# Optimization experiments

Hardware: AMD Instinct MI355X
Metric: run time of the kernel (lower is better)

The kernel has to match this reference:

```python
import jax, jax.numpy as jnp
import numpy as np

N_SAMPLES = 16384
SPB = 1024            # samples_per_block
ROOM = (16, 16, 16)   # room_dim
MIC = (8, 8, 8)       # mic_location
ENV_SIZE = 16         # impulse_envelope_size
N_BLOCKS = N_SAMPLES // SPB
N_COEFFS = SPB // 2 + 1


def _linear_interp(env, out_size):
    # torch F.interpolate(mode='linear', align_corners=False) along last axis
    in_size = env.shape[-1]
    scale = in_size / out_size
    coords = jnp.clip((jnp.arange(out_size, dtype=jnp.float32) + 0.5) * scale - 0.5,
                      0.0, in_size - 1.0)
    lo = jnp.floor(coords).astype(jnp.int32)
    hi = jnp.minimum(lo + 1, in_size - 1)
    w = coords - lo.astype(jnp.float32)
    return env[..., lo] * (1.0 - w) + env[..., hi] * w


def setup_inputs() -> dict:
    key = jax.random.key(0)
    k1, k2, k3, k4 = jax.random.split(key, 4)
    x = jax.random.normal(k1, (1, 1, N_SAMPLES), dtype=jnp.float32)  # unused by forward
    transfer_functions = jax.random.uniform(k2, (N_BLOCKS, *ROOM, N_COEFFS), dtype=jnp.float32)
    impulses = jax.random.uniform(k3, (N_BLOCKS, *ROOM, ENV_SIZE), dtype=jnp.float32)
    # the torch forward draws U(-1,1) noise each block; hoisted here as an input
    noise = jax.random.uniform(k4, (N_BLOCKS, *ROOM, SPB), minval=-1.0, maxval=1.0,
                               dtype=jnp.float32)
    return {"x": x, "transfer_functions": transfer_functions,
            "impulses": impulses, "noise": noise}


def reference(x, transfer_functions, impulses, noise):
    # Precompute per-block excitation envelopes: interp -> clamp -> * noise
    env = jnp.clip(_linear_interp(impulses, SPB), 0.0, 1.0) * noise  # (B, X, Y, Z, T)
    res = jnp.clip(transfer_functions, 0.0, 1.0)                      # (B, X, Y, Z, F)

    def step(sound_field, blk):
        e, r = blk
        sf = sound_field + e
        spec = jnp.fft.rfft(sf, axis=-1, norm='ortho')
        sf = jnp.fft.irfft(r * spec, n=SPB, axis=-1, norm='ortho')
        mic = sf[MIC[0], MIC[1], MIC[2]]                              # (T,)
        # 3x3x3 ones-kernel box sum over spatial dims, zero padding 1 (== unfold path)
        sf = jax.lax.reduce_window(sf, 0.0, jax.lax.add,
                                   (3, 3, 3, 1), (1, 1, 1, 1), 'SAME')
        return sf, mic

    sf0 = jnp.zeros((*ROOM, SPB), dtype=jnp.float32)
    _, mics = jax.lax.scan(step, sf0, (env, res))                     # mics: (B, T)
    return mics.reshape(-1, 1, N_SAMPLES)                             # (1, 1, n_samples)
```

## Files before the change

### kernel.cpp

```cpp
#include <hip/hip_runtime.h>


#define NFFT   1024
#define NF     513
#define NKP    257
#define NCELLS 4096
#define NPAIR  2048
#define PI2    6.28318530717958647692f
#define RT2    0.70710678118654752f

__device__ __forceinline__ int SW(int i) {
    return i ^ ((i >> 4) & 7) ^ ((i >> 7) & 7);
}
__device__ __forceinline__ int slotof(int k) {
    return ((k & 7) << 7) | (((k >> 3) & 7) << 4) | (((k >> 6) & 7) << 1) | ((k >> 9) & 1);
}
__device__ __forceinline__ float clip01(float v) { return fminf(fmaxf(v, 0.0f), 1.0f); }
__device__ __forceinline__ unsigned pkh2(float a, float b) {
    union { _Float16 h[2]; unsigned u; } z;
    z.h[0] = (_Float16)a; z.h[1] = (_Float16)b;
    return z.u;
}
__device__ __forceinline__ float h2lo(unsigned u) {
    union { unsigned u; _Float16 h[2]; } z; z.u = u; return (float)z.h[0];
}
__device__ __forceinline__ float h2hi(unsigned u) {
    union { unsigned u; _Float16 h[2]; } z; z.u = u; return (float)z.h[1];
}
__device__ __forceinline__ unsigned cmp4(const uint4& v, int c) {
    return c == 0 ? v.x : c == 1 ? v.y : c == 2 ? v.z : v.w;
}
__device__ __forceinline__ float4 f4add(float4 a, float4 b) {
    return make_float4(a.x + b.x, a.y + b.y, a.z + b.z, a.w + b.w);
}
__device__ __forceinline__ float4 f4sub(float4 a, float4 b) {
    return make_float4(a.x - b.x, a.y - b.y, a.z - b.z, a.w - b.w);
}
__device__ __forceinline__ float4 cmul2(float4 d, float2 w) {
    return make_float4(d.x * w.x - d.y * w.y, d.x * w.y + d.y * w.x,
                       d.z * w.x - d.w * w.y, d.z * w.y + d.w * w.x);
}
__device__ __forceinline__ float4 nI(float4 v) { return make_float4(v.y, -v.x, v.w, -v.z); }
__device__ __forceinline__ float4 pI(float4 v) { return make_float4(-v.y, v.x, -v.w, v.z); }
__device__ __forceinline__ float4 w81(float4 v) {
    return make_float4(RT2 * (v.x + v.y), RT2 * (v.y - v.x),
                       RT2 * (v.z + v.w), RT2 * (v.w - v.z));
}
__device__ __forceinline__ float4 w83(float4 v) {
    return make_float4(RT2 * (v.y - v.x), RT2 * (-v.x - v.y),
                       RT2 * (v.w - v.z), RT2 * (-v.z - v.w));
}

__device__ __forceinline__ void dft8(float4* a) {
    float4 c0 = f4add(a[0], a[4]), c1 = f4add(a[1], a[5]);
    float4 c2 = f4add(a[2], a[6]), c3 = f4add(a[3], a[7]);
    float4 d0 = f4sub(a[0], a[4]);
    float4 d1 = w81(f4sub(a[1], a[5]));
    float4 d2 = nI (f4sub(a[2], a[6]));
    float4 d3 = w83(f4sub(a[3], a[7]));
    float4 t0 = f4add(c0, c2), t1 = f4add(c1, c3);
    float4 t2 = f4sub(c0, c2), t3 = f4sub(c1, c3);
    float4 s0 = f4add(d0, d2), s1 = f4add(d1, d3);
    float4 s2 = f4sub(d0, d2), s3 = f4sub(d1, d3);
    a[0] = f4add(t0, t1);      a[4] = f4sub(t0, t1);
    a[2] = f4add(t2, nI(t3));  a[6] = f4add(t2, pI(t3));
    a[1] = f4add(s0, s1);      a[5] = f4sub(s0, s1);
    a[3] = f4add(s2, nI(s3));  a[7] = f4add(s2, pI(s3));
}

__device__ __forceinline__ void twiddle7(float4* a, int j, float invL) {
    float sv, cv;
    __sincosf(-PI2 * (float)j * invL, &sv, &cv);
    float2 w1 = make_float2(cv, sv), wp = w1;
    a[1] = cmul2(a[1], wp);
    #pragma unroll
    for (int p = 2; p < 8; ++p) {
        wp = make_float2(wp.x * w1.x - wp.y * w1.y, wp.x * w1.y + wp.y * w1.x);
        a[p] = cmul2(a[p], wp);
    }
}

__global__ __launch_bounds__(256, 5) void k_p1(
    const float* __restrict__ tf, const float* __restrict__ imp,
    const float* __restrict__ noise, unsigned* __restrict__ Et,
    unsigned* __restrict__ TFt)
{
    __shared__ float4 FD[2][1024];

    const int tid = threadIdx.x;
    const int bid = blockIdx.x;
    const int w   = ((bid & 7) << 10) | (bid >> 3);
    const int b   = w >> 9;
    const int c0  = (w & 511) << 3;
    const int buf = tid >> 7, j1 = tid & 127;
    const int cb  = c0 + 4 * buf;

    {
        const float* nz = noise + ((size_t)b * NCELLS + cb) * (size_t)NFFT;
        float nzv[32];
        #pragma unroll
        for (int m = 0; m < 8; ++m) {
            #pragma unroll
            for (int cc = 0; cc < 4; ++cc)
                nzv[4 * m + cc] = nz[cc * NFFT + j1 + (m << 7)];
        }
        const float* ipr = imp + ((size_t)b * NCELLS + cb) * 16;
        float4 a[8];
        #pragma unroll
        for (int m = 0; m < 8; ++m) {
            int n = j1 + (m << 7);
            float coord = (n + 0.5f) * (16.0f / 1024.0f) - 0.5f;
            coord = fminf(fmaxf(coord, 0.0f), 15.0f);
            int lo = (int)coord;
            int hi = lo + 1 > 15 ? 15 : lo + 1;
            float wl = coord - (float)lo, wh = 1.0f - wl;
            float4 e;
            e.x = clip01(ipr[lo]      * wh + ipr[hi]      * wl) * nzv[4 * m + 0];
            e.y = clip01(ipr[16 + lo] * wh + ipr[16 + hi] * wl) * nzv[4 * m + 1];
            e.z = clip01(ipr[32 + lo] * wh + ipr[32 + hi] * wl) * nzv[4 * m + 2];
            e.w = clip01(ipr[48 + lo] * wh + ipr[48 + hi] * wl) * nzv[4 * m + 3];
            a[m] = e;
        }
        dft8(a);
        twiddle7(a, j1, 1.0f / 1024.0f);
        #pragma unroll
        for (int p = 0; p < 8; ++p) FD[buf][SW(j1 + (p << 7))] = a[p];
    }
    __syncthreads();

    {
        const int idx0 = ((j1 >> 4) << 7) + (j1 & 15);
        float4 a[8];
        #pragma unroll
        for (int m = 0; m < 8; ++m) a[m] = FD[buf][SW(idx0 + (m << 4))];
        dft8(a);
        twiddle7(a, j1 & 15, 1.0f / 128.0f);
        #pragma unroll
        for (int p = 0; p < 8; ++p) FD[buf][SW(idx0 + (p << 4))] = a[p];
    }
    __syncthreads();

    {
        const int idx0 = ((j1 >> 1) << 4) + (j1 & 1);
        float4 a[8];
        #pragma unroll
        for (int m = 0; m < 8; ++m) a[m] = FD[buf][SW(idx0 + (m << 1))];
        dft8(a);
        twiddle7(a, j1 & 1, 1.0f / 16.0f);
        #pragma unroll
        for (int p = 0; p < 8; ++p) FD[buf][SW(idx0 + (p << 1))] = a[p];
    }
    __syncthreads();

    #pragma unroll
    for (int it = 0; it < 2; ++it) {
        int p = tid + (it << 8);
        float4 A0 = FD[0][SW(2 * p)], B0 = FD[0][SW(2 * p + 1)];
        float4 A1 = FD[1][SW(2 * p)], B1 = FD[1][SW(2 * p + 1)];
        float4 y00 = f4add(A0, B0), y10 = f4sub(A0, B0);
        float4 y01 = f4add(A1, B1), y11 = f4sub(A1, B1);
        uint4 u0 = { pkh2(y00.x, y00.y), pkh2(y00.z, y00.w),
                     pkh2(y01.x, y01.y), pkh2(y01.z, y01.w) };
        uint4 u1 = { pkh2(y10.x, y10.y), pkh2(y10.z, y10.w),
                     pkh2(y11.x, y11.y), pkh2(y11.z, y11.w) };
        unsigned* base = Et + ((size_t)b * NFFT + 2 * p) * NPAIR + (c0 >> 1);
        *(uint4*)base = u0;
        *(uint4*)(base + NPAIR) = u1;
    }

    {
        const float* r_[8];
        #pragma unroll
        for (int cc = 0; cc < 8; ++cc)
            r_[cc] = tf + ((size_t)b * NCELLS + c0 + cc) * NF;
        for (int kp = tid; kp < NKP; kp += 256) {
            bool hv = kp < 256;
            uint4 ua, ub;
            ua.x = pkh2(clip01(r_[0][2 * kp]), hv ? clip01(r_[0][2 * kp + 1]) : 0.0f);
            ua.y = pkh2(clip01(r_[1][2 * kp]), hv ? clip01(r_[1][2 * kp + 1]) : 0.0f);
            ua.z = pkh2(clip01(r_[2][2 * kp]), hv ? clip01(r_[2][2 * kp + 1]) : 0.0f);
            ua.w = pkh2(clip01(r_[3][2 * kp]), hv ? clip01(r_[3][2 * kp + 1]) : 0.0f);
            ub.x = pkh2(clip01(r_[4][2 * kp]), hv ? clip01(r_[4][2 * kp + 1]) : 0.0f);
            ub.y = pkh2(clip01(r_[5][2 * kp]), hv ? clip01(r_[5][2 * kp + 1]) : 0.0f);
            ub.z = pkh2(clip01(r_[6][2 * kp]), hv ? clip01(r_[6][2 * kp + 1]) : 0.0f);
            ub.w = pkh2(clip01(r_[7][2 * kp]), hv ? clip01(r_[7][2 * kp + 1]) : 0.0f);
            unsigned* dst = TFt + ((size_t)b * NKP + kp) * NCELLS + c0;
            *(uint4*)dst = ua;
            *(uint4*)(dst + 4) = ub;
        }
    }
}

__global__ __launch_bounds__(1024, 8) void k_p2(
    const unsigned* __restrict__ Et, const unsigned* __restrict__ TFt,
    float2* __restrict__ ms)
{
    __shared__ float2 Sz[4096];

    const int q    = threadIdx.x;
    const int lane = q & 63;
    const int k    = blockIdx.x;
    const bool dual = (k == 0);
    const int kp  = dual ? 0 : (k >> 1);
    const int sel = dual ? 0 : (k & 1);
    const int rA  = dual ? 0 : slotof(k);
    const int rB  = dual ? 1 : slotof((1024 - k) & 1023);
    const int x = q >> 6, y = (q >> 2) & 15, zs = (q & 3) << 2;

    #define AX(qq, dz) (((qq) << 2) | ((dz) ^ ((qq) & 3) ^ (((qq) >> 2) & 3)))

    float2 SF[4];
    #pragma unroll
    for (int dz = 0; dz < 4; ++dz) SF[dz] = make_float2(0.f, 0.f);

    #pragma unroll 1
    for (int b = 0; b < 16; ++b) {
        const uint2 ea = *(const uint2*)(Et + ((size_t)b * NFFT + rA) * NPAIR + 2 * q);
        const uint2 eb = *(const uint2*)(Et + ((size_t)b * NFFT + rB) * NPAIR + 2 * q);
        const uint4 tp = *(const uint4*)(TFt + ((size_t)b * NKP + kp) * NCELLS + 4 * q);
        uint4 tp2;
        if (dual) tp2 = *(const uint4*)(TFt + ((size_t)b * NKP + 256) * NCELLS + 4 * q);

        float2 T[4];
        if (!dual) {
            #pragma unroll
            for (int j = 0; j < 2; ++j) {
                unsigned fu = j ? ea.y : ea.x;
                unsigned gu = j ? eb.y : eb.x;
                float fr = h2lo(fu), fi = h2hi(fu);
                float gr = h2lo(gu), gi = h2hi(gu);
                float ear = 0.5f * (fr + gr), eai = 0.5f * (fi - gi);
                float ebr = 0.5f * (fi + gi), ebi = 0.5f * (gr - fr);
                unsigned te = cmp4(tp, 2 * j);
                unsigned to = cmp4(tp, 2 * j + 1);
                float re_ = sel ? h2hi(te) : h2lo(te);
                float ro_ = sel ? h2hi(to) : h2lo(to);
                T[2 * j]     = make_float2(re_ * (SF[2 * j].x + ear),
                                           re_ * (SF[2 * j].y + eai));
                T[2 * j + 1] = make_float2(ro_ * (SF[2 * j + 1].x + ebr),
                                           ro_ * (SF[2 * j + 1].y + ebi));
            }
        } else {
            #pragma unroll
            for (int dz = 0; dz < 4; ++dz) {
                unsigned fu = (dz >> 1) ? ea.y : ea.x;
                unsigned gu = (dz >> 1) ? eb.y : eb.x;
                float e0   = (dz & 1) ? h2hi(fu) : h2lo(fu);
                float e512 = (dz & 1) ? h2hi(gu) : h2lo(gu);
                float tA = h2lo(cmp4(tp, dz));
                float tB = h2lo(cmp4(tp2, dz));
                T[dz] = make_float2(tA * (SF[dz].x + e0),
                                    tB * (SF[dz].y + e512));
            }
        }
        if (q == 546) {
            if (dual) {
                ms[b * NF + 0]   = make_float2(T[0].x, 0.0f);
                ms[b * NF + 512] = make_float2(T[0].y, 0.0f);
            } else {
                ms[b * NF + k] = T[0];
            }
        }

        float2 D, U;
        D.x = __shfl(T[3].x, lane - 1, 64); D.y = __shfl(T[3].y, lane - 1, 64);
        U.x = __shfl(T[0].x, lane + 1, 64); U.y = __shfl(T[0].y, lane + 1, 64);
        float2 Z[4];
        Z[0] = make_float2(T[0].x + T[1].x + (zs > 0 ? D.x : 0.f),
                           T[0].y + T[1].y + (zs > 0 ? D.y : 0.f));
        Z[1] = make_float2(T[0].x + T[1].x + T[2].x, T[0].y + T[1].y + T[2].y);
        Z[2] = make_float2(T[1].x + T[2].x + T[3].x, T[1].y + T[2].y + T[3].y);
        Z[3] = make_float2(T[2].x + T[3].x + (zs < 12 ? U.x : 0.f),
                           T[2].y + T[3].y + (zs < 12 ? U.y : 0.f));

        #pragma unroll
        for (int dz = 0; dz < 4; ++dz) Sz[AX(q, dz)] = Z[dz];
        __syncthreads();
        #pragma unroll
        for (int dz = 0; dz < 4; ++dz) {
            float2 s = Z[dz];
            if (y > 0)  { float2 u = Sz[AX(q - 4, dz)]; s.x += u.x; s.y += u.y; }
            if (y < 15) { float2 u = Sz[AX(q + 4, dz)]; s.x += u.x; s.y += u.y; }
            Z[dz] = s;
        }
        __syncthreads();
        #pragma unroll
        for (int dz = 0; dz < 4; ++dz) Sz[AX(q, dz)] = Z[dz];
        __syncthreads();
        #pragma unroll
        for (int dz = 0; dz < 4; ++dz) {
            float2 s = Z[dz];
            if (x > 0)  { float2 u = Sz[AX(q - 64, dz)]; s.x += u.x; s.y += u.y; }
            if (x < 15) { float2 u = Sz[AX(q + 64, dz)]; s.x += u.x; s.y += u.y; }
            SF[dz] = s;
        }
        __syncthreads();
    }
    #undef AX
}

__device__ __forceinline__ int pd(int i) { return i + (i >> 5); }

__global__ __launch_bounds__(256) void k_p3(
    const float2* __restrict__ ms, float* __restrict__ out)
{
    __shared__ float2 FD[1056];
    const int b = blockIdx.x, tid = threadIdx.x;

    for (int j = tid; j < NFFT; j += 256) {
        int jj = (j <= 512) ? j : 1024 - j;
        float2 v = ms[b * NF + jj];
        if (j > 512) v.y = -v.y;
        FD[pd(__brev(j) >> 22)] = v;
    }
    __syncthreads();

    for (int lg = 0; lg <= 9; ++lg) {
        const int len = 1 << lg;
        for (int pr = tid; pr < 512; pr += 256) {
            const int jj = pr & (len - 1);
            const int i0 = ((pr >> lg) << (lg + 1)) + jj;
            const int i1 = i0 + len;
            const int iw = jj << (9 - lg);
            float sn, cs;
            __sincosf(-PI2 * (1.0f / 1024.0f) * (float)iw, &sn, &cs);
            float2 a = FD[pd(i0)], bb = FD[pd(i1)];
            float tr = bb.x * cs + bb.y * sn;
            float ti = bb.y * cs - bb.x * sn;
            FD[pd(i0)] = make_float2(a.x + tr, a.y + ti);
            FD[pd(i1)] = make_float2(a.x - tr, a.y - ti);
        }
        __syncthreads();
    }
    for (int t = tid; t < NFFT; t += 256)
        out[b * NFFT + t] = FD[pd(t)].x * (1.0f / 1024.0f);
}

extern "C" void kernel_launch(void* const* d_in, const int* in_sizes, int n_in,
                              void* d_out, int out_size, void* d_ws, size_t ws_size,
                              hipStream_t stream)
{
    const float* tf    = (const float*)d_in[1];
    const float* imp   = (const float*)d_in[2];
    const float* noise = (const float*)d_in[3];
    float* out = (float*)d_out;

    unsigned* Et  = (unsigned*)d_ws;
    unsigned* TFt = Et + (size_t)16 * NFFT * NPAIR;
    float2*   ms  = (float2*)(TFt + (size_t)16 * NKP * NCELLS);

    k_p1<<<8192, 256, 0, stream>>>(tf, imp, noise, Et, TFt);
    k_p2<<<512, 1024, 0, stream>>>(Et, TFt, ms);
    k_p3<<<16, 256, 0, stream>>>(ms, out);
}
```

Measured before the change: 264.4 us.

## Stage FFT output in shared memory and write Et in contiguous cell-chunk layout

Each k_p1 block now handles 16 cells, in two passes of 8, instead of 8. Spectra are staged in a padded shared-memory buffer, and Et is rewritten into a chunked layout [b][cellchunk][freq][8] so each block writes one contiguous 32KB region instead of scattered 16-byte pieces across rows. k_p2 indexing is updated to match. The cost is fewer blocks, more shared memory (occupancy hint cut from 5 to 2), and k_p2 reads that are now less contiguous per wavefront (8-byte pieces spread across chunks).

```diff
diff --git a/kernel.cpp b/kernel.cpp
--- a/kernel.cpp
+++ b/kernel.cpp
@@ -5,7 +5,6 @@
 #define NF     513
 #define NKP    257
 #define NCELLS 4096
-#define NPAIR  2048
 #define PI2    6.28318530717958647692f
 #define RT2    0.70710678118654752f
 
@@ -80,113 +79,146 @@
     }
 }
 
-__global__ __launch_bounds__(256, 5) void k_p1(
+__global__ __launch_bounds__(256, 2) void k_p1(
     const float* __restrict__ tf, const float* __restrict__ imp,
     const float* __restrict__ noise, unsigned* __restrict__ Et,
     unsigned* __restrict__ TFt)
 {
     __shared__ float4 FD[2][1024];
+    __shared__ unsigned stag[1024 * 9];
 
     const int tid = threadIdx.x;
     const int bid = blockIdx.x;
-    const int w   = ((bid & 7) << 10) | (bid >> 3);
-    const int b   = w >> 9;
-    const int c0  = (w & 511) << 3;
+    const int w   = ((bid & 7) << 9) | (bid >> 3);
+    const int b   = w >> 8;
+    const int c0  = (w & 255) << 4;
     const int buf = tid >> 7, j1 = tid & 127;
-    const int cb  = c0 + 4 * buf;
-
+
+    float2 tu0[3], tu1[3], tl[3];
     {
-        const float* nz = noise + ((size_t)b * NCELLS + cb) * (size_t)NFFT;
-        float nzv[32];
-        #pragma unroll
-        for (int m = 0; m < 8; ++m) {
-            #pragma unroll
-            for (int cc = 0; cc < 4; ++cc)
-                nzv[4 * m + cc] = nz[cc * NFFT + j1 + (m << 7)];
-        }
-        const float* ipr = imp + ((size_t)b * NCELLS + cb) * 16;
-        float4 a[8];
-        #pragma unroll
-        for (int m = 0; m < 8; ++m) {
-            int n = j1 + (m << 7);
-            float coord = (n + 0.5f) * (16.0f / 1024.0f) - 0.5f;
-            coord = fminf(fmaxf(coord, 0.0f), 15.0f);
-            int lo = (int)coord;
-            int hi = lo + 1 > 15 ? 15 : lo + 1;
-            float wl = coord - (float)lo, wh = 1.0f - wl;
-            float4 e;
-            e.x = clip01(ipr[lo]      * wh + ipr[hi]      * wl) * nzv[4 * m + 0];
-            e.y = clip01(ipr[16 + lo] * wh + ipr[16 + hi] * wl) * nzv[4 * m + 1];
-            e.z = clip01(ipr[32 + lo] * wh + ipr[32 + hi] * wl) * nzv[4 * m + 2];
-            e.w = clip01(ipr[48 + lo] * wh + ipr[48 + hi] * wl) * nzv[4 * m + 3];
-            a[m] = e;
-        }
-        dft8(a);
-        twiddle7(a, j1, 1.0f / 1024.0f);
-        #pragma unroll
-        for (int p = 0; p < 8; ++p) FD[buf][SW(j1 + (p << 7))] = a[p];
+        float s, c;
+        __sincosf(-PI2 * (1.0f / 1024.0f) * (float)j1, &s, &c);           tu0[0] = make_float2(c, s);
+        __sincosf(-PI2 * (1.0f / 1024.0f) * (float)(j1 & 15), &s, &c);
+        tu0[1] = make_float2(c, s);
+        __sincosf(-PI2 * (1.0f / 1024.0f) * (float)(j1 & 1), &s, &c);
+        tu0[2] = make_float2(c, s);
+    }
+
+    #pragma unroll 1
+    for (int bb = 0; bb < 2; ++bb) {
+        const int cb = c0 + 8 * bb + 4 * buf;
+        if (bb) __syncthreads();
+
+        {
+            const float* nz = noise + ((size_t)b * NCELLS + cb) * (size_t)NFFT;
+            float nzv[32];
+            #pragma unroll
+            for (int m = 0; m < 8; ++m) {
+                #pragma unroll
+                for (int cc = 0; cc < 4; ++cc)
+                    nzv[4 * m + cc] = nz[cc * NFFT + j1 + (m << 7)];
+            }
+            const float* ipr = imp + ((size_t)b * NCELLS + cb) * 16;
+            float4 a[8];
+            #pragma unroll
+            for (int m = 0; m < 8; ++m) {
+                int n = j1 + (m << 7);
+                float coord = (n + 0.5f) * (16.0f / 1024.0f) - 0.5f;
+                coord = fminf(fmaxf(coord, 0.0f), 15.0f);
+                int lo = (int)coord;
+                int hi = lo + 1 > 15 ? 15 : lo + 1;
+                float wl = coord - (float)lo, wh = 1.0f - wl;
+                float4 e;
+                e.x = clip01(ipr[lo]      * wh + ipr[hi]      * wl) * nzv[4 * m + 0];
+                e.y = clip01(ipr[16 + lo] * wh + ipr[16 + hi] * wl) * nzv[4 * m + 1];
+                e.z = clip01(ipr[32 + lo] * wh + ipr[32 + hi] * wl) * nzv[4 * m + 2];
+                e.w = clip01(ipr[48 + lo] * wh + ipr[48 + hi] * wl) * nzv[4 * m + 3];
+                a[m] = e;
+            }
+            dft8(a);
+            twiddle7(a, j1, 1.0f / 1024.0f);
+            #pragma unroll
+            for (int p = 0; p < 8; ++p) FD[buf][SW(j1 + (p << 7))] = a[p];
+        }
+        __syncthreads();
+
+        {
+            const int idx0 = ((j1 >> 4) << 7) + (j1 & 15);
+            float4 a[8];
+            #pragma unroll
+            for (int m = 0; m < 8; ++m) a[m] = FD[buf][SW(idx0 + (m << 4))];
+            dft8(a);
+            twiddle7(a, j1 & 15, 1.0f / 128.0f);
+            #pragma unroll
+            for (int p = 0; p < 8; ++p) FD[buf][SW(idx0 + (p << 4))] = a[p];
+        }
+        __syncthreads();
+
+        {
+            const int idx0 = ((j1 >> 1) << 4) + (j1 & 1);
+            float4 a[8];
+            #pragma unroll
+            for (int m = 0; m < 8; ++m) a[m] = FD[buf][SW(idx0 + (m << 1))];
+            dft8(a);
+            twiddle7(a, j1 & 1, 1.0f / 16.0f);
+            #pragma unroll
+            for (int p = 0; p < 8; ++p) FD[buf][SW(idx0 + (p << 1))] = a[p];
+        }
+        __syncthreads();
+
+        #pragma unroll
+        for (int it = 0; it < 2; ++it) {
+            int p = tid + (it << 8);
+            float4 A0 = FD[0][SW(2 * p)], B0 = FD[0][SW(2 * p + 1)];
+            float4 A1 = FD[1][SW(2 * p)], B1 = FD[1][SW(2 * p + 1)];
+            float4 y00 = f4add(A0, B0), y10 = f4sub(A0, B0);
+            float4 y01 = f4add(A1, B1), y11 = f4sub(A1, B1);
+            int r0 = (2 * p) * 9 + 4 * bb;
+            int r1 = (2 * p + 1) * 9 + 4 * bb;
+            stag[r0 + 0] = pkh2(y00.x, y00.y);
+            stag[r0 + 1] = pkh2(y00.z, y00.w);
+            stag[r0 + 2] = pkh2(y01.x, y01.y);
+            stag[r0 + 3] = pkh2(y01.z, y01.w);
+            stag[r1 + 0] = pkh2(y10.x, y10.y);
+            stag[r1 + 1] = pkh2(y10.z, y10.w);
+            stag[r1 + 2] = pkh2(y11.x, y11.y);
+            stag[r1 + 3] = pkh2(y11.z, y11.w);
+        }
     }
     __syncthreads();
 
     {
-        const int idx0 = ((j1 >> 4) << 7) + (j1 & 15);
-        float4 a[8];
-        #pragma unroll
-        for (int m = 0; m < 8; ++m) a[m] = FD[buf][SW(idx0 + (m << 4))];
-        dft8(a);
-        twiddle7(a, j1 & 15, 1.0f / 128.0f);
-        #pragma unroll
-        for (int p = 0; p < 8; ++p) FD[buf][SW(idx0 + (p << 4))] = a[p];
-    }
-    __syncthreads();
+        unsigned* base = Et + (((size_t)b * 256 + (c0 >> 4)) * 1024) * 8;
+        #pragma unroll
+        for (int it = 0; it < 4; ++it) {
+            int s = tid + (it << 8);
+            uint4 lo = { stag[s * 9 + 0], stag[s * 9 + 1], stag[s * 9 + 2], stag[s * 9 + 3] };
+            uint4 hi = { stag[s * 9 + 4], stag[s * 9 + 5], stag[s * 9 + 6], stag[s * 9 + 7] };
+            *(uint4*)(base + (size_t)s * 8)     = lo;
+            *(uint4*)(base + (size_t)s * 8 + 4) = hi;
+        }
+    }
 
     {
-        const int idx0 = ((j1 >> 1) << 4) + (j1 & 1);
-        float4 a[8];
-        #pragma unroll
-        for (int m = 0; m < 8; ++m) a[m] = FD[buf][SW(idx0 + (m << 1))];
-        dft8(a);
-        twiddle7(a, j1 & 1, 1.0f / 16.0f);
-        #pragma unroll
-        for (int p = 0; p < 8; ++p) FD[buf][SW(idx0 + (p << 1))] = a[p];
-    }
-    __syncthreads();
-
-    #pragma unroll
-    for (int it = 0; it < 2; ++it) {
-        int p = tid + (it << 8);
-        float4 A0 = FD[0][SW(2 * p)], B0 = FD[0][SW(2 * p + 1)];
-        float4 A1 = FD[1][SW(2 * p)], B1 = FD[1][SW(2 * p + 1)];
-        float4 y00 = f4add(A0, B0), y10 = f4sub(A0, B0);
-        float4 y01 = f4add(A1, B1), y11 = f4sub(A1, B1);
-        uint4 u0 = { pkh2(y00.x, y00.y), pkh2(y00.z, y00.w),
-                     pkh2(y01.x, y01.y), pkh2(y01.z, y01.w) };
-        uint4 u1 = { pkh2(y10.x, y10.y), pkh2(y10.z, y10.w),
-                     pkh2(y11.x, y11.y), pkh2(y11.z, y11.w) };
-        unsigned* base = Et + ((size_t)b * NFFT + 2 * p) * NPAIR + (c0 >> 1);
-        *(uint4*)base = u0;
-        *(uint4*)(base + NPAIR) = u1;
-    }
-
-    {
-        const float* r_[8];
-        #pragma unroll
-        for (int cc = 0; cc < 8; ++cc)
-            r_[cc] = tf + ((size_t)b * NCELLS + c0 + cc) * NF;
+        const float* rbase = tf + ((size_t)b * NCELLS + c0) * NF;
         for (int kp = tid; kp < NKP; kp += 256) {
             bool hv = kp < 256;
-            uint4 ua, ub;
-            ua.x = pkh2(clip01(r_[0][2 * kp]), hv ? clip01(r_[0][2 * kp + 1]) : 0.0f);
-            ua.y = pkh2(clip01(r_[1][2 * kp]), hv ? clip01(r_[1][2 * kp + 1]) : 0.0f);
-            ua.z = pkh2(clip01(r_[2][2 * kp]), hv ? clip01(r_[2][2 * kp + 1]) : 0.0f);
-            ua.w = pkh2(clip01(r_[3][2 * kp]), hv ? clip01(r_[3][2 * kp + 1]) : 0.0f);
-            ub.x = pkh2(clip01(r_[4][2 * kp]), hv ? clip01(r_[4][2 * kp + 1]) : 0.0f);
-            ub.y = pkh2(clip01(r_[5][2 * kp]), hv ? clip01(r_[5][2 * kp + 1]) : 0.0f);
-            ub.z = pkh2(clip01(r_[6][2 * kp]), hv ? clip01(r_[6][2 * kp + 1]) : 0.0f);
-            ub.w = pkh2(clip01(r_[7][2 * kp]), hv ? clip01(r_[7][2 * kp + 1]) : 0.0f);
+            uint4 u[4];
+            #pragma unroll
+            for (int g = 0; g < 4; ++g) {
+                unsigned vv[4];
+                #pragma unroll
+                for (int cq = 0; cq < 4; ++cq) {
+                    const float* rr = rbase + (size_t)(4 * g + cq) * NF;
+                    vv[cq] = pkh2(clip01(rr[2 * kp]), hv ? clip01(rr[2 * kp + 1]) : 0.0f);
+                }
+                u[g] = make_uint4(vv[0], vv[1], vv[2], vv[3]);
+            }
             unsigned* dst = TFt + ((size_t)b * NKP + kp) * NCELLS + c0;
-            *(uint4*)dst = ua;
-            *(uint4*)(dst + 4) = ub;
+            *(uint4*)(dst)      = u[0];
+            *(uint4*)(dst + 4)  = u[1];
+            *(uint4*)(dst + 8)  = u[2];
+            *(uint4*)(dst + 12) = u[3];
         }
     }
 }
@@ -215,8 +247,9 @@
 
     #pragma unroll 1
     for (int b = 0; b < 16; ++b) {
-        const uint2 ea = *(const uint2*)(Et + ((size_t)b * NFFT + rA) * NPAIR + 2 * q);
-        const uint2 eb = *(const uint2*)(Et + ((size_t)b * NFFT + rB) * NPAIR + 2 * q);
+        const size_t chunkbase = ((size_t)b * 256 + (q >> 2)) * 1024;
+        const uint2 ea = *(const uint2*)(Et + (chunkbase + rA) * 8 + 2 * (q & 3));
+        const uint2 eb = *(const uint2*)(Et + (chunkbase + rB) * 8 + 2 * (q & 3));
         const uint4 tp = *(const uint4*)(TFt + ((size_t)b * NKP + kp) * NCELLS + 4 * q);
         uint4 tp2;
         if (dual) tp2 = *(const uint4*)(TFt + ((size_t)b * NKP + 256) * NCELLS + 4 * q);
@@ -346,10 +379,10 @@
     float* out = (float*)d_out;
 
     unsigned* Et  = (unsigned*)d_ws;
-    unsigned* TFt = Et + (size_t)16 * NFFT * NPAIR;
+    unsigned* TFt = Et + (size_t)16 * 256 * 1024 * 8;
     float2*   ms  = (float2*)(TFt + (size_t)16 * NKP * NCELLS);
 
-    k_p1<<<8192, 256, 0, stream>>>(tf, imp, noise, Et, TFt);
+    k_p1<<<4096, 256, 0, stream>>>(tf, imp, noise, Et, TFt);
     k_p2<<<512, 1024, 0, stream>>>(Et, TFt, ms);
     k_p3<<<16, 256, 0, stream>>>(ms, out);
 }
```

New measurement: 313.1 us. 18.4% more time.

## Switch forward FFT to radix-4 with one 4-cell group per block

Applied to the files above, without the earlier changes.

The first-stage kernel moves from a 3-pass radix-8 FFT (two 4-cell groups per 256-thread block, with a final radix-2 pass) to a 5-pass radix-4 FFT over a single 4-cell group per block. The block count doubles, the shared-memory buffer halves and the XOR swizzle is dropped. The output slot mapping changes to a base-4 digit reversal, and the consumer kernel's index function is updated to match. The aim is higher occupancy and lower register pressure in exchange for more passes and barriers, possible unswizzled LDS bank conflicts, and narrower scattered global stores.

```diff
diff --git a/kernel.cpp b/kernel.cpp
--- a/kernel.cpp
+++ b/kernel.cpp
@@ -7,13 +7,10 @@
 #define NCELLS 4096
 #define NPAIR  2048
 #define PI2    6.28318530717958647692f
-#define RT2    0.70710678118654752f
-
-__device__ __forceinline__ int SW(int i) {
-    return i ^ ((i >> 4) & 7) ^ ((i >> 7) & 7);
-}
-__device__ __forceinline__ int slotof(int k) {
-    return ((k & 7) << 7) | (((k >> 3) & 7) << 4) | (((k >> 6) & 7) << 1) | ((k >> 9) & 1);
+
+__device__ __forceinline__ int slotof4(int k) {
+    return ((k & 3) << 8) | (((k >> 2) & 3) << 6) | (((k >> 4) & 3) << 4) |
+           (((k >> 6) & 3) << 2) | ((k >> 8) & 3);
 }
 __device__ __forceinline__ float clip01(float v) { return fminf(fmaxf(v, 0.0f), 1.0f); }
 __device__ __forceinline__ unsigned pkh2(float a, float b) {
@@ -42,73 +39,54 @@
 }
 __device__ __forceinline__ float4 nI(float4 v) { return make_float4(v.y, -v.x, v.w, -v.z); }
 __device__ __forceinline__ float4 pI(float4 v) { return make_float4(-v.y, v.x, -v.w, v.z); }
-__device__ __forceinline__ float4 w81(float4 v) {
-    return make_float4(RT2 * (v.x + v.y), RT2 * (v.y - v.x),
-                       RT2 * (v.z + v.w), RT2 * (v.w - v.z));
-}
-__device__ __forceinline__ float4 w83(float4 v) {
-    return make_float4(RT2 * (v.y - v.x), RT2 * (-v.x - v.y),
-                       RT2 * (v.w - v.z), RT2 * (-v.z - v.w));
-}
-
-__device__ __forceinline__ void dft8(float4* a) {
-    float4 c0 = f4add(a[0], a[4]), c1 = f4add(a[1], a[5]);
-    float4 c2 = f4add(a[2], a[6]), c3 = f4add(a[3], a[7]);
-    float4 d0 = f4sub(a[0], a[4]);
-    float4 d1 = w81(f4sub(a[1], a[5]));
-    float4 d2 = nI (f4sub(a[2], a[6]));
-    float4 d3 = w83(f4sub(a[3], a[7]));
-    float4 t0 = f4add(c0, c2), t1 = f4add(c1, c3);
-    float4 t2 = f4sub(c0, c2), t3 = f4sub(c1, c3);
-    float4 s0 = f4add(d0, d2), s1 = f4add(d1, d3);
-    float4 s2 = f4sub(d0, d2), s3 = f4sub(d1, d3);
-    a[0] = f4add(t0, t1);      a[4] = f4sub(t0, t1);
-    a[2] = f4add(t2, nI(t3));  a[6] = f4add(t2, pI(t3));
-    a[1] = f4add(s0, s1);      a[5] = f4sub(s0, s1);
-    a[3] = f4add(s2, nI(s3));  a[7] = f4add(s2, pI(s3));
-}
-
-__device__ __forceinline__ void twiddle7(float4* a, int j, float invL) {
+
+__device__ __forceinline__ void dft4(float4* a) {
+    float4 e = f4add(a[0], a[2]), f = f4add(a[1], a[3]);
+    float4 g = f4sub(a[0], a[2]), h = f4sub(a[1], a[3]);
+    a[0] = f4add(e, f);
+    a[2] = f4sub(e, f);
+    a[1] = f4add(g, nI(h));
+    a[3] = f4add(g, pI(h));
+}
+
+__device__ __forceinline__ void twiddle3(float4* a, int j, float invL) {
     float sv, cv;
     __sincosf(-PI2 * (float)j * invL, &sv, &cv);
     float2 w1 = make_float2(cv, sv), wp = w1;
     a[1] = cmul2(a[1], wp);
-    #pragma unroll
-    for (int p = 2; p < 8; ++p) {
-        wp = make_float2(wp.x * w1.x - wp.y * w1.y, wp.x * w1.y + wp.y * w1.x);
-        a[p] = cmul2(a[p], wp);
-    }
-}
-
-__global__ __launch_bounds__(256, 5) void k_p1(
+    wp = make_float2(wp.x * w1.x - wp.y * w1.y, wp.x * w1.y + wp.y * w1.x);
+    a[2] = cmul2(a[2], wp);
+    wp = make_float2(wp.x * w1.x - wp.y * w1.y, wp.x * w1.y + wp.y * w1.x);
+    a[3] = cmul2(a[3], wp);
+}
+
+__global__ __launch_bounds__(256, 8) void k_p1(
     const float* __restrict__ tf, const float* __restrict__ imp,
     const float* __restrict__ noise, unsigned* __restrict__ Et,
     unsigned* __restrict__ TFt)
 {
-    __shared__ float4 FD[2][1024];
+    __shared__ float4 FD[1024];
 
     const int tid = threadIdx.x;
     const int bid = blockIdx.x;
-    const int w   = ((bid & 7) << 10) | (bid >> 3);
-    const int b   = w >> 9;
-    const int c0  = (w & 511) << 3;
-    const int buf = tid >> 7, j1 = tid & 127;
-    const int cb  = c0 + 4 * buf;
+    const int w   = ((bid & 7) << 11) | (bid >> 3);
+    const int b   = w >> 10;
+    const int c0  = (w & 1023) << 2;
 
     {
-        const float* nz = noise + ((size_t)b * NCELLS + cb) * (size_t)NFFT;
-        float nzv[32];
-        #pragma unroll
-        for (int m = 0; m < 8; ++m) {
+        const float* nz = noise + ((size_t)b * NCELLS + c0) * (size_t)NFFT;
+        float nzv[16];
+        #pragma unroll
+        for (int m = 0; m < 4; ++m) {
             #pragma unroll
             for (int cc = 0; cc < 4; ++cc)
-                nzv[4 * m + cc] = nz[cc * NFFT + j1 + (m << 7)];
-        }
-        const float* ipr = imp + ((size_t)b * NCELLS + cb) * 16;
-        float4 a[8];
-        #pragma unroll
-        for (int m = 0; m < 8; ++m) {
-            int n = j1 + (m << 7);
+                nzv[4 * m + cc] = nz[cc * NFFT + tid + (m << 8)];
+        }
+        const float* ipr = imp + ((size_t)b * NCELLS + c0) * 16;
+        float4 a[4];
+        #pragma unroll
+        for (int m = 0; m < 4; ++m) {
+            int n = tid + (m << 8);
             float coord = (n + 0.5f) * (16.0f / 1024.0f) - 0.5f;
             coord = fminf(fmaxf(coord, 0.0f), 15.0f);
             int lo = (int)coord;
@@ -121,72 +99,64 @@
             e.w = clip01(ipr[48 + lo] * wh + ipr[48 + hi] * wl) * nzv[4 * m + 3];
             a[m] = e;
         }
-        dft8(a);
-        twiddle7(a, j1, 1.0f / 1024.0f);
-        #pragma unroll
-        for (int p = 0; p < 8; ++p) FD[buf][SW(j1 + (p << 7))] = a[p];
+        dft4(a);
+        twiddle3(a, tid, 1.0f / 1024.0f);
+        #pragma unroll
+        for (int p = 0; p < 4; ++p) FD[tid + (p << 8)] = a[p];
     }
     __syncthreads();
 
+    #pragma unroll
+    for (int pi = 0; pi < 3; ++pi) {
+        const int lgs = 6 - 2 * pi;
+        const int s   = 1 << lgs;
+        const int j   = tid & (s - 1);
+        const int idx0 = ((tid >> lgs) << (lgs + 2)) | j;
+        float4 a[4];
+        #pragma unroll
+        for (int m = 0; m < 4; ++m) a[m] = FD[idx0 + (m << lgs)];
+        dft4(a);
+        twiddle3(a, j, 1.0f / (float)(s << 2));
+        #pragma unroll
+        for (int p = 0; p < 4; ++p) FD[idx0 + (p << lgs)] = a[p];
+        __syncthreads();
+    }
+
     {
-        const int idx0 = ((j1 >> 4) << 7) + (j1 & 15);
-        float4 a[8];
-        #pragma unroll
-        for (int m = 0; m < 8; ++m) a[m] = FD[buf][SW(idx0 + (m << 4))];
-        dft8(a);
-        twiddle7(a, j1 & 15, 1.0f / 128.0f);
-        #pragma unroll
-        for (int p = 0; p < 8; ++p) FD[buf][SW(idx0 + (p << 4))] = a[p];
+        const int idx0 = tid << 2;
+        float4 a[4];
+        #pragma unroll
+        for (int m = 0; m < 4; ++m) a[m] = FD[idx0 + m];
+        dft4(a);
+        #pragma unroll
+        for (int p = 0; p < 4; ++p) FD[idx0 + p] = a[p];
     }
     __syncthreads();
 
     {
-        const int idx0 = ((j1 >> 1) << 4) + (j1 & 1);
-        float4 a[8];
-        #pragma unroll
-        for (int m = 0; m < 8; ++m) a[m] = FD[buf][SW(idx0 + (m << 1))];
-        dft8(a);
-        twiddle7(a, j1 & 1, 1.0f / 16.0f);
-        #pragma unroll
-        for (int p = 0; p < 8; ++p) FD[buf][SW(idx0 + (p << 1))] = a[p];
-    }
-    __syncthreads();
-
-    #pragma unroll
-    for (int it = 0; it < 2; ++it) {
-        int p = tid + (it << 8);
-        float4 A0 = FD[0][SW(2 * p)], B0 = FD[0][SW(2 * p + 1)];
-        float4 A1 = FD[1][SW(2 * p)], B1 = FD[1][SW(2 * p + 1)];
-        float4 y00 = f4add(A0, B0), y10 = f4sub(A0, B0);
-        float4 y01 = f4add(A1, B1), y11 = f4sub(A1, B1);
-        uint4 u0 = { pkh2(y00.x, y00.y), pkh2(y00.z, y00.w),
-                     pkh2(y01.x, y01.y), pkh2(y01.z, y01.w) };
-        uint4 u1 = { pkh2(y10.x, y10.y), pkh2(y10.z, y10.w),
-                     pkh2(y11.x, y11.y), pkh2(y11.z, y11.w) };
-        unsigned* base = Et + ((size_t)b * NFFT + 2 * p) * NPAIR + (c0 >> 1);
-        *(uint4*)base = u0;
-        *(uint4*)(base + NPAIR) = u1;
+        unsigned* base = Et + (size_t)b * NFFT * NPAIR + (c0 >> 1);
+        #pragma unroll
+        for (int it = 0; it < 4; ++it) {
+            int s = tid + (it << 8);
+            float4 v = FD[s];
+            uint2 u = { pkh2(v.x, v.y), pkh2(v.z, v.w) };
+            *(uint2*)(base + (size_t)s * NPAIR) = u;
+        }
     }
 
     {
-        const float* r_[8];
-        #pragma unroll
-        for (int cc = 0; cc < 8; ++cc)
-            r_[cc] = tf + ((size_t)b * NCELLS + c0 + cc) * NF;
+        const float* r0 = tf + ((size_t)b * NCELLS + c0) * NF;
+        const float* r1 = r0 + NF;
+        const float* r2 = r1 + NF;
+        const float* r3 = r2 + NF;
         for (int kp = tid; kp < NKP; kp += 256) {
             bool hv = kp < 256;
-            uint4 ua, ub;
-            ua.x = pkh2(clip01(r_[0][2 * kp]), hv ? clip01(r_[0][2 * kp + 1]) : 0.0f);
-            ua.y = pkh2(clip01(r_[1][2 * kp]), hv ? clip01(r_[1][2 * kp + 1]) : 0.0f);
-            ua.z = pkh2(clip01(r_[2][2 * kp]), hv ? clip01(r_[2][2 * kp + 1]) : 0.0f);
-            ua.w = pkh2(clip01(r_[3][2 * kp]), hv ? clip01(r_[3][2 * kp + 1]) : 0.0f);
-            ub.x = pkh2(clip01(r_[4][2 * kp]), hv ? clip01(r_[4][2 * kp + 1]) : 0.0f);
-            ub.y = pkh2(clip01(r_[5][2 * kp]), hv ? clip01(r_[5][2 * kp + 1]) : 0.0f);
-            ub.z = pkh2(clip01(r_[6][2 * kp]), hv ? clip01(r_[6][2 * kp + 1]) : 0.0f);
-            ub.w = pkh2(clip01(r_[7][2 * kp]), hv ? clip01(r_[7][2 * kp + 1]) : 0.0f);
-            unsigned* dst = TFt + ((size_t)b * NKP + kp) * NCELLS + c0;
-            *(uint4*)dst = ua;
-            *(uint4*)(dst + 4) = ub;
+            uint4 u;
+            u.x = pkh2(clip01(r0[2 * kp]), hv ? clip01(r0[2 * kp + 1]) : 0.0f);
+            u.y = pkh2(clip01(r1[2 * kp]), hv ? clip01(r1[2 * kp + 1]) : 0.0f);
+            u.z = pkh2(clip01(r2[2 * kp]), hv ? clip01(r2[2 * kp + 1]) : 0.0f);
+            u.w = pkh2(clip01(r3[2 * kp]), hv ? clip01(r3[2 * kp + 1]) : 0.0f);
+            *(uint4*)(TFt + ((size_t)b * NKP + kp) * NCELLS + c0) = u;
         }
     }
 }
@@ -203,8 +173,8 @@
     const bool dual = (k == 0);
     const int kp  = dual ? 0 : (k >> 1);
     const int sel = dual ? 0 : (k & 1);
-    const int rA  = dual ? 0 : slotof(k);
-    const int rB  = dual ? 1 : slotof((1024 - k) & 1023);
+    const int rA  = slotof4(dual ? 0 : k);
+    const int rB  = slotof4(dual ? 512 : ((1024 - k) & 1023));
     const int x = q >> 6, y = (q >> 2) & 15, zs = (q & 3) << 2;
 
     #define AX(qq, dz) (((qq) << 2) | ((dz) ^ ((qq) & 3) ^ (((qq) >> 2) & 3)))
@@ -349,7 +319,7 @@
     unsigned* TFt = Et + (size_t)16 * NFFT * NPAIR;
     float2*   ms  = (float2*)(TFt + (size_t)16 * NKP * NCELLS);
 
-    k_p1<<<8192, 256, 0, stream>>>(tf, imp, noise, Et, TFt);
+    k_p1<<<16384, 256, 0, stream>>>(tf, imp, noise, Et, TFt);
     k_p2<<<512, 1024, 0, stream>>>(Et, TFt, ms);
     k_p3<<<16, 256, 0, stream>>>(ms, out);
 }
```

Measured after the change: 284.5 us. +7.6%, slower.
